# Performance work log

Hardware: AMD Instinct MI355X
Metric: run time of the kernel (lower is better)

Reference implementation:

```python
import jax, jax.numpy as jnp
import numpy as np

B, L, D, H = 8, 512, 1024, 16
HD = D // H  # head dim = 64
SCALE = 1.0  # scale=False in __init__


def _rel_sinusoid(seq_len, dim):
    # RelativeSinusoidalPositionalEmbedding lookup for relative positions
    # arange(-L/2, L/2) (even L), sinusoid of the raw relative position.
    half = dim // 2
    inv = jnp.exp(jnp.arange(half, dtype=jnp.float32) * (-(np.log(10000.0) / (half - 1))))
    r = jnp.arange(-(seq_len // 2), seq_len // 2, dtype=jnp.float32)  # (L,)
    ang = r[:, None] * inv[None, :]  # (L, half)
    return jnp.concatenate([jnp.sin(ang), jnp.cos(ang)], axis=1)  # (L, dim)


def setup_inputs() -> dict:
    key = jax.random.key(0)
    ks = jax.random.split(key, 8)
    s = 0.02
    x = jax.random.normal(ks[0], (B, L, D), jnp.float32)
    mask = jax.random.randint(ks[1], (B, L), 0, 2).astype(jnp.int64)
    mask = mask.at[:, 0].set(1)  # ensure at least one valid key per row
    qmask = jax.random.randint(ks[2], (B, L), 0, 2).astype(jnp.int64)
    w_qkv = jax.random.normal(ks[3], (D, 3 * D), jnp.float32) * s
    w_qkpos = jax.random.normal(ks[4], (HD, 2 * D), jnp.float32) * s
    w_fc = jax.random.normal(ks[5], (D, D), jnp.float32) * s
    b_fc = jnp.zeros((D,), jnp.float32)
    shift = jnp.abs(jax.random.normal(ks[6], (1,), jnp.float32)) + 0.001
    bias = -jnp.abs(jax.random.normal(ks[7], (1,), jnp.float32))
    return dict(x=x, mask=mask, qmask=qmask, w_qkv=w_qkv, w_qkpos=w_qkpos,
                w_fc=w_fc, b_fc=b_fc, shift=shift, bias=bias)


def reference(x, mask, qmask, w_qkv, w_qkpos, w_fc, b_fc, shift, bias):
    # trans_type='self', use_Gaussian=True, dropout in eval mode (identity)
    b, l, d = x.shape
    qkv = x @ w_qkv  # (B, L, 3D)
    q, k, v = jnp.split(qkv, 3, axis=-1)
    q = q.reshape(b, l, H, HD).transpose(0, 2, 1, 3)  # (B,H,L,hd)
    k = k.reshape(b, l, H, HD).transpose(0, 2, 1, 3)
    v = v.reshape(b, l, H, HD).transpose(0, 2, 1, 3)

    pe = _rel_sinusoid(l, HD)               # (L, hd)
    y = pe @ w_qkpos                        # (L, 2D)
    q_p, k_p = jnp.split(y, 2, axis=-1)     # (L, D) each
    q_p = q_p.reshape(l, H, HD).transpose(1, 0, 2)  # (H, L, hd)
    k_p = k_p.reshape(l, H, HD).transpose(1, 0, 2)  # (H, L, hd)

    attn = jnp.einsum('bhid,bhjd->bhij', q, k) + jnp.einsum('hid,hjd->hij', q_p, k_p)[None]

    # speaker-identity masking: zero out cross-speaker scores (trans_type='self')
    qsame = qmask[:, :, None] == qmask[:, None, :]  # (B, L, L)
    attn = jnp.where(qsame[:, None], attn, 0.0)
    attn = attn / SCALE

    # key padding mask -> -inf
    attn = jnp.where(mask[:, None, None, :] == 0, -jnp.inf, attn)

    # Gaussian distance bias: -(shift * (i-j)^2 + bias)
    idx = jnp.arange(l, dtype=jnp.float32)
    sqd = (idx[:, None] - idx[None, :]) ** 2  # (L, L)
    attn = attn + (-(shift[0] * sqd + bias[0]))[None, None]

    attn = jax.nn.softmax(attn, axis=-1)
    out = jnp.einsum('bhij,bhjd->bhid', attn, v)  # (B,H,L,hd)
    out = out.transpose(0, 2, 1, 3).reshape(b, l, d)
    return out @ w_fc + b_fc
```

## Files before the change

### kernel.cpp

```cpp
#include <hip/hip_runtime.h>
#include <hip/hip_bf16.h>

#define BB 8
#define LL 512
#define DD 1024
#define HH 16
#define HD 64
#define LOG2E 1.4426950408889634f

typedef __attribute__((ext_vector_type(8))) unsigned short u16x8;
typedef __attribute__((ext_vector_type(4))) unsigned short u16x4;
typedef __attribute__((ext_vector_type(8))) __bf16 bf16x8;
typedef __attribute__((ext_vector_type(4))) float f32x4;
typedef __attribute__((ext_vector_type(16))) float f32x16;

#define DEV __device__ __forceinline__

DEV unsigned short f2bf(float f) {
    return __builtin_bit_cast(unsigned short, (__bf16)f);
}
DEV f32x4 mfma16(u16x8 a, u16x8 b, f32x4 c) {
    return __builtin_amdgcn_mfma_f32_16x16x32_bf16(
        __builtin_bit_cast(bf16x8, a), __builtin_bit_cast(bf16x8, b), c, 0, 0, 0);
}
DEV f32x16 mfma32(u16x8 a, u16x8 b, f32x16 c) {
    return __builtin_amdgcn_mfma_f32_32x32x16_bf16(
        __builtin_bit_cast(bf16x8, a), __builtin_bit_cast(bf16x8, b), c, 0, 0, 0);
}
typedef __attribute__((address_space(1))) void gv_t;
typedef __attribute__((address_space(3))) void lv_t;
DEV void gload16(const void* g, void* l) {
    __builtin_amdgcn_global_load_lds((gv_t*)g, (lv_t*)l, 16, 0, 0);
}


__global__ __launch_bounds__(256) void cvt_x(const float* __restrict__ in,
                                             unsigned short* __restrict__ out) {
    int i = blockIdx.x * 256 + threadIdx.x;
    f32x4 v = *(const f32x4*)(in + i * 4);
    u16x4 o;
    o[0] = f2bf(v[0]); o[1] = f2bf(v[1]); o[2] = f2bf(v[2]); o[3] = f2bf(v[3]);
    *(u16x4*)(out + i * 4) = o;
}

__global__ __launch_bounds__(256) void transpose_cvt(
    const float* __restrict__ in, unsigned short* __restrict__ out,
    int R, int C) {
    __shared__ unsigned short tile[32][33];
    int c0 = blockIdx.x * 32, r0 = blockIdx.y * 32;
    int tx = threadIdx.x & 31, ty = threadIdx.x >> 5;
#pragma unroll
    for (int i = 0; i < 32; i += 8)
        tile[ty + i][tx] = f2bf(in[(r0 + ty + i) * C + c0 + tx]);
    __syncthreads();
#pragma unroll
    for (int i = 0; i < 32; i += 8)
        out[(c0 + ty + i) * R + r0 + tx] = tile[tx][ty + i];
}

__global__ __launch_bounds__(256) void posg(
    const float* __restrict__ w, unsigned short* __restrict__ qpx,
    unsigned short* __restrict__ kpx) {
    __shared__ float peS[64][64];
    __shared__ float wS[64][32];
    int c0 = blockIdx.x * 32, i0 = blockIdx.y * 64;
    int t = threadIdx.x;
#pragma unroll
    for (int j = 0; j < 16; ++j) {
        int o = t + j * 256;
        int ri = o >> 6, d = o & 63, dd = d & 31;
        float inv = expf((float)dd * -0.2971077539347156f);
        float ang = (float)(i0 + ri - 256) * inv;
        peS[ri][d] = (d < 32) ? sinf(ang) : cosf(ang);
    }
#pragma unroll
    for (int j = 0; j < 8; ++j) {
        int o = t + j * 256;
        wS[o >> 5][o & 31] = w[(o >> 5) * 2048 + c0 + (o & 31)];
    }
    __syncthreads();
#pragma unroll
    for (int j = 0; j < 8; ++j) {
        int o = t + j * 256;
        int row = o >> 5, col = o & 31;
        float acc = 0.0f;
#pragma unroll
        for (int k = 0; k < 64; ++k) acc += peS[row][k] * wS[k][col];
        int c = c0 + col, i = i0 + row;
        int qt = i >> 5, lq = i & 31;
        int cc = (c < 1024) ? c : (c - 1024);
        int h = cc >> 6, kk = cc & 63;
        int ks = kk >> 4, h2 = (kk >> 3) & 1, jj = kk & 7;
        unsigned idx = ((unsigned)(h * 4096 + qt * 256 + ks * 64 + h2 * 32 + lq)
                        << 3) + jj;
        if (c < 1024) qpx[idx] = f2bf(acc * LOG2E);
        else          kpx[idx] = f2bf(acc);
    }
}

template <int MODE>
__global__ __launch_bounds__(256) void gemm_bt(
    const unsigned short* __restrict__ A, const unsigned short* __restrict__ Bt,
    int M, int N, int K, int NBX, unsigned short* __restrict__ o0,
    unsigned short* __restrict__ o1, unsigned short* __restrict__ o2,
    float* __restrict__ fout, const float* __restrict__ bias) {
    __shared__ __align__(16) unsigned short As[2][128 * 32];
    __shared__ __align__(16) unsigned short Bs[2][128 * 32];
    int g = blockIdx.x;
    int swz = (g & 7) * (gridDim.x >> 3) + (g >> 3);
    int bx = swz % NBX, by = swz / NBX;
    int m0 = by * 128, n0 = bx * 128;
    int t = threadIdx.x;
    int w = t >> 6, l = t & 63, lg = l >> 4, lc = l & 15;
    int wr = w >> 1, wc = w & 1;

    f32x4 acc[4][4] = {};

    int sr = t >> 2;
    int sc = (t & 3) ^ ((t >> 3) & 3);
    const unsigned short* Ab = A + (m0 + sr) * K + sc * 8;
    const unsigned short* Bb = Bt + (n0 + sr) * K + sc * 8;
    int rsw = (lc >> 1) & 3;

    auto stage = [&](int buf, int k0) {
        gload16(Ab + k0, &As[buf][w * 512]);
        gload16(Ab + 64 * K + k0, &As[buf][2048 + w * 512]);
        gload16(Bb + k0, &Bs[buf][w * 512]);
        gload16(Bb + 64 * K + k0, &Bs[buf][2048 + w * 512]);
    };

    stage(0, 0);
    stage(1, 32);
    int cur = 0;
    for (int k0 = 0; k0 < K; k0 += 32) {
        if (k0 + 32 < K)
            asm volatile("s_waitcnt vmcnt(4)" ::: "memory");
        else
            asm volatile("s_waitcnt vmcnt(0)" ::: "memory");
        __builtin_amdgcn_sched_barrier(0);
        __builtin_amdgcn_s_barrier();
        __builtin_amdgcn_sched_barrier(0);
        u16x8 af[4], bf[4];
#pragma unroll
        for (int mm = 0; mm < 4; ++mm)
            af[mm] = *(const u16x8*)&As[cur][(wr * 64 + mm * 16 + lc) * 32 +
                                             ((lg ^ rsw) << 3)];
#pragma unroll
        for (int nn = 0; nn < 4; ++nn)
            bf[nn] = *(const u16x8*)&Bs[cur][(wc * 64 + nn * 16 + lc) * 32 +
                                             ((lg ^ rsw) << 3)];
        asm volatile("s_waitcnt lgkmcnt(0)" ::: "memory");
        __builtin_amdgcn_sched_barrier(0);
        __builtin_amdgcn_s_barrier();
        __builtin_amdgcn_sched_barrier(0);
        if (k0 + 64 < K) stage(cur, k0 + 64);
#pragma unroll
        for (int mm = 0; mm < 4; ++mm)
#pragma unroll
            for (int nn = 0; nn < 4; ++nn)
                acc[mm][nn] = mfma16(af[mm], bf[nn], acc[mm][nn]);
        cur ^= 1;
    }

#pragma unroll
    for (int mm = 0; mm < 4; ++mm)
#pragma unroll
        for (int nn = 0; nn < 4; ++nn)
#pragma unroll
            for (int r = 0; r < 4; ++r) {
                int row = m0 + wr * 64 + mm * 16 + lg * 4 + r;
                int col = n0 + wc * 64 + nn * 16 + lc;
                float v = acc[mm][nn][r];
                if (MODE == 0) {
                    int bb = row >> 9, i = row & 511;
                    int which = col >> 10, dd = col & 1023;
                    int hh = dd >> 6, hd = dd & 63;
                    int bh2 = bb * HH + hh;
                    int tl = i >> 5, io = i & 31;
                    if (which == 2) {
                        int h2 = (io >> 2) & 1, ps = (io >> 4) & 1;
                        int j = (io & 3) | (((io >> 3) & 1) << 2);
                        int dblk = hd >> 5, lq = hd & 31;
                        unsigned idx = ((unsigned)(bh2 * 4096 + tl * 256 +
                                        (dblk * 2 + ps) * 64 + h2 * 32 + lq)
                                        << 3) + j;
                        o2[idx] = f2bf(v);
                    } else {
                        int ks = hd >> 4, h2 = (hd >> 3) & 1, j = hd & 7;
                        unsigned idx = ((unsigned)(bh2 * 4096 + tl * 256 +
                                        ks * 64 + h2 * 32 + io) << 3) + j;
                        if (which == 0) o0[idx] = f2bf(v * LOG2E);
                        else            o1[idx] = f2bf(v);
                    }
                } else {
                    fout[row * N + col] = v + bias[col];
                }
            }
}

__global__ void attn_k(
    const unsigned short* __restrict__ Qx, const unsigned short* __restrict__ Kx,
    const unsigned short* __restrict__ Vx, const unsigned short* __restrict__ QPx,
    const unsigned short* __restrict__ KPx, const int* __restrict__ mask,
    const int* __restrict__ qmask, const float* __restrict__ shp,
    unsigned short* __restrict__ out) {
    __shared__ float mbuf[2][64];
    __shared__ float lsbuf[2][64];
    __shared__ float obuf[2][64][33];

    int g = blockIdx.x;
    int bid = ((g & 7) << 7) + (g >> 3);
    int b = bid >> 7, h = (bid >> 3) & 15, qc = bid & 7;
    int t = threadIdx.x, w = t >> 6, l = t & 63;
    int qg = w & 1, kh = w >> 1;
    int lq = l & 31, hi = l >> 5;
    int q = qc * 64 + qg * 32 + lq;
    int bh = b * HH + h;
    int qt = qc * 2 + qg;

    const unsigned short* qb  = Qx  + (((unsigned)(bh * 4096 + qt * 256)) << 3) + (l << 3);
    const unsigned short* qpb = QPx + (((unsigned)(h  * 4096 + qt * 256)) << 3) + (l << 3);
    u16x8 qf[4], pf[4];
#pragma unroll
    for (int ks = 0; ks < 4; ++ks) {
        qf[ks] = *(const u16x8*)(qb + ks * 512);
        pf[ks] = *(const u16x8*)(qpb + ks * 512);
    }

    unsigned long long km[4], qm[4];
#pragma unroll
    for (int t8 = 0; t8 < 4; ++t8) {
        int base = b * LL + (kh * 4 + t8) * 64 + l;
        km[t8] = __ballot(mask[base] != 0);
        qm[t8] = __ballot(qmask[base] != 0);
    }
    int qi = (qmask[b * LL + q] != 0) ? 1 : 0;

    const float M0 = -1.0e30f, NEGF = -3.0e38f, THR = 8.0f;
    float negs = -(*shp) * LOG2E;
    float m = M0, ls = 0.0f;
    f32x16 o0 = {}, o1 = {};
    float fq = (float)(q - 4 * hi);

#pragma unroll
    for (int tt = 0; tt < 8; ++tt) {
        int ttg = kh * 8 + tt;
        const unsigned short* kb  = Kx  + (((unsigned)(bh * 4096 + ttg * 256)) << 3) + (l << 3);
        const unsigned short* kpb = KPx + (((unsigned)(h  * 4096 + ttg * 256)) << 3) + (l << 3);
        const unsigned short* vb  = Vx  + (((unsigned)(bh * 4096 + ttg * 256)) << 3) + (l << 3);
        u16x8 vf0 = *(const u16x8*)(vb);
        u16x8 vf1 = *(const u16x8*)(vb + 512);
        u16x8 vf2 = *(const u16x8*)(vb + 1024);
        u16x8 vf3 = *(const u16x8*)(vb + 1536);
        f32x16 sk = {}, sp = {};
#pragma unroll
        for (int ks = 0; ks < 4; ++ks) {
            sk = mfma32(*(const u16x8*)(kb + ks * 512), qf[ks], sk);
            sp = mfma32(*(const u16x8*)(kpb + ks * 512), pf[ks], sp);
        }

        unsigned kwn = ((unsigned)(km[tt >> 1] >> ((tt & 1) * 32))) >> (hi * 4);
        unsigned qwn = ((unsigned)(qm[tt >> 1] >> ((tt & 1) * 32))) >> (hi * 4);
        float bt = fq - 32.0f * (float)ttg;
        float p[16];
#pragma unroll
        for (int r = 0; r < 16; ++r) {
            const int off = (r & 3) + 8 * (r >> 2);
            float v = sk[r] + sp[r];
            v = (((qwn >> off) & 1u) == (unsigned)qi) ? v : 0.0f;
            float dr = bt - (float)off;
            v = __builtin_fmaf(negs * dr, dr, v);
            v = ((kwn >> off) & 1u) ? v : NEGF;
            p[r] = v;
        }
        float a0 = fmaxf(fmaxf(p[0], p[1]), fmaxf(p[2], p[3]));
        float a1 = fmaxf(fmaxf(p[4], p[5]), fmaxf(p[6], p[7]));
        float a2 = fmaxf(fmaxf(p[8], p[9]), fmaxf(p[10], p[11]));
        float a3 = fmaxf(fmaxf(p[12], p[13]), fmaxf(p[14], p[15]));
        float pmax = fmaxf(fmaxf(a0, a1), fmaxf(a2, a3));
        pmax = fmaxf(pmax, __shfl_xor(pmax, 32));
        if (!__all(pmax <= m + THR)) {
            float mn = fmaxf(m, pmax);
            float sc = __builtin_amdgcn_exp2f(m - mn);
#pragma unroll
            for (int r = 0; r < 16; ++r) { o0[r] *= sc; o1[r] *= sc; }
            ls *= sc;
            m = mn;
        }
#pragma unroll
        for (int r = 0; r < 16; ++r) p[r] = __builtin_amdgcn_exp2f(p[r] - m);
        ls += (((p[0] + p[1]) + (p[2] + p[3])) + ((p[4] + p[5]) + (p[6] + p[7]))) +
              (((p[8] + p[9]) + (p[10] + p[11])) +
               ((p[12] + p[13]) + (p[14] + p[15])));
        u16x8 pf0, pf1;
#pragma unroll
        for (int j = 0; j < 8; ++j) { pf0[j] = f2bf(p[j]); pf1[j] = f2bf(p[8 + j]); }
        o0 = mfma32(vf0, pf0, o0);
        o0 = mfma32(vf1, pf1, o0);
        o1 = mfma32(vf2, pf0, o1);
        o1 = mfma32(vf3, pf1, o1);
    }

    if (kh == 1) {
        mbuf[qg][l] = m;
        lsbuf[qg][l] = ls;
#pragma unroll
        for (int r = 0; r < 16; ++r) {
            obuf[qg][l][r] = o0[r];
            obuf[qg][l][16 + r] = o1[r];
        }
    }
    __syncthreads();
    if (kh == 0) {
        float m1 = mbuf[qg][l], ls1 = lsbuf[qg][l];
        float mm = fmaxf(m, m1);
        float sc0 = __builtin_amdgcn_exp2f(m - mm);
        float sc1 = __builtin_amdgcn_exp2f(m1 - mm);
        float lsm = ls * sc0 + ls1 * sc1;
        float rs = lsm + __shfl_xor(lsm, 32);
        float rinv = __builtin_amdgcn_rcpf(rs);
        unsigned short* ob = out + ((long)(b * LL + q)) * DD + h * HD + hi * 4;
#pragma unroll
        for (int rg = 0; rg < 4; ++rg) {
            u16x4 pk0, pk1;
#pragma unroll
            for (int rr = 0; rr < 4; ++rr) {
                int i = rg * 4 + rr;
                float v0 = __builtin_fmaf(o0[i], sc0, obuf[qg][l][i] * sc1);
                float v1 = __builtin_fmaf(o1[i], sc0, obuf[qg][l][16 + i] * sc1);
                pk0[rr] = f2bf(v0 * rinv);
                pk1[rr] = f2bf(v1 * rinv);
            }
            *(u16x4*)(ob + rg * 8) = pk0;
            *(u16x4*)(ob + 32 + rg * 8) = pk1;
        }
    }
}

extern "C" void kernel_launch(void* const* d_in, const int* in_sizes, int n_in,
                              void* d_out, int out_size, void* d_ws,
                              size_t ws_size, hipStream_t stream) {
    const float* x     = (const float*)d_in[0];
    const int*   mask  = (const int*)d_in[1];
    const int*   qmask = (const int*)d_in[2];
    const float* w_qkv = (const float*)d_in[3];
    const float* w_qkp = (const float*)d_in[4];
    const float* w_fc  = (const float*)d_in[5];
    const float* b_fc  = (const float*)d_in[6];
    const float* shift = (const float*)d_in[7];

    char* ws = (char*)d_ws;
    unsigned short* xb   = (unsigned short*)(ws);
    unsigned short* qb   = (unsigned short*)(ws + 8388608);
    unsigned short* kb   = (unsigned short*)(ws + 16777216);
    unsigned short* vtb  = (unsigned short*)(ws + 25165824);
    unsigned short* qp   = (unsigned short*)(ws + 33554432);
    unsigned short* kp   = (unsigned short*)(ws + 34603008);
    unsigned short* wqt  = (unsigned short*)(ws + 35651584);
    unsigned short* wft  = (unsigned short*)(ws + 41943040);
    unsigned short* aout = (unsigned short*)(ws + 44040192);

    cvt_x<<<4096, 256, 0, stream>>>(x, xb);
    transpose_cvt<<<dim3(96, 32), 256, 0, stream>>>(w_qkv, wqt, 1024, 3072);
    transpose_cvt<<<dim3(32, 32), 256, 0, stream>>>(w_fc, wft, 1024, 1024);
    posg<<<dim3(64, 8), 256, 0, stream>>>(w_qkp, qp, kp);
    gemm_bt<0><<<768, 256, 0, stream>>>(xb, wqt, 4096, 3072, 1024, 24, qb, kb,
                                        vtb, nullptr, nullptr);
    attn_k<<<1024, 256, 0, stream>>>(qb, kb, vtb, qp, kp, mask, qmask, shift,
                                     aout);
    gemm_bt<1><<<256, 256, 0, stream>>>(aout, wft, 4096, 1024, 1024, 8, nullptr,
                                        nullptr, nullptr, (float*)d_out, b_fc);
}
```

Measured before the change: 136.2 us.

## Process two query tiles per wave in attention to reuse K/V loads

Each wave now handles two 32-row query tiles instead of one, so every K, K-positional and V fragment loaded from global memory is used for two score and PV MFMA chains. The grid is halved to 512 blocks and the shared-memory reduction buffers are doubled to hold both tiles' partial softmax states. The aim is to cut redundant global K/V traffic and give the scheduler more independent MFMA work. The cost is higher register pressure, which may lower occupancy, and fewer blocks to spread across CUs.

```diff
diff --git a/kernel.cpp b/kernel.cpp
--- a/kernel.cpp
+++ b/kernel.cpp
@@ -204,27 +204,29 @@
     const unsigned short* __restrict__ KPx, const int* __restrict__ mask,
     const int* __restrict__ qmask, const float* __restrict__ shp,
     unsigned short* __restrict__ out) {
-    __shared__ float mbuf[2][64];
-    __shared__ float lsbuf[2][64];
-    __shared__ float obuf[2][64][33];
+    __shared__ float mbuf[2][2][64];
+    __shared__ float lsbuf[2][2][64];
+    __shared__ float obuf[2][2][64][33];
 
     int g = blockIdx.x;
-    int bid = ((g & 7) << 7) + (g >> 3);
-    int b = bid >> 7, h = (bid >> 3) & 15, qc = bid & 7;
+    int bid = ((g & 7) << 6) + (g >> 3);
+    int b = bid >> 6, h = (bid >> 2) & 15, qq = bid & 3;
     int t = threadIdx.x, w = t >> 6, l = t & 63;
     int qg = w & 1, kh = w >> 1;
     int lq = l & 31, hi = l >> 5;
-    int q = qc * 64 + qg * 32 + lq;
+    int c0 = qq * 4 + qg * 2, c1 = c0 + 1;
+    int qA = c0 * 32 + lq, qB = qA + 32;
     int bh = b * HH + h;
-    int qt = qc * 2 + qg;
-
-    const unsigned short* qb  = Qx  + (((unsigned)(bh * 4096 + qt * 256)) << 3) + (l << 3);
-    const unsigned short* qpb = QPx + (((unsigned)(h  * 4096 + qt * 256)) << 3) + (l << 3);
-    u16x8 qf[4], pf[4];
+
+    const unsigned short* qbA  = Qx  + (((unsigned)(bh * 4096 + c0 * 256)) << 3) + (l << 3);
+    const unsigned short* qpbA = QPx + (((unsigned)(h  * 4096 + c0 * 256)) << 3) + (l << 3);
+    u16x8 qfA[4], pfA[4], qfB[4], pfB[4];
 #pragma unroll
     for (int ks = 0; ks < 4; ++ks) {
-        qf[ks] = *(const u16x8*)(qb + ks * 512);
-        pf[ks] = *(const u16x8*)(qpb + ks * 512);
+        qfA[ks] = *(const u16x8*)(qbA + ks * 512);
+        pfA[ks] = *(const u16x8*)(qpbA + ks * 512);
+        qfB[ks] = *(const u16x8*)(qbA + 2048 + ks * 512);
+        pfB[ks] = *(const u16x8*)(qpbA + 2048 + ks * 512);
     }
 
     unsigned long long km[4], qm[4];
@@ -234,13 +236,15 @@
         km[t8] = __ballot(mask[base] != 0);
         qm[t8] = __ballot(qmask[base] != 0);
     }
-    int qi = (qmask[b * LL + q] != 0) ? 1 : 0;
+    int qiA = (qmask[b * LL + qA] != 0) ? 1 : 0;
+    int qiB = (qmask[b * LL + qB] != 0) ? 1 : 0;
 
     const float M0 = -1.0e30f, NEGF = -3.0e38f, THR = 8.0f;
     float negs = -(*shp) * LOG2E;
-    float m = M0, ls = 0.0f;
-    f32x16 o0 = {}, o1 = {};
-    float fq = (float)(q - 4 * hi);
+    float mA = M0, lsA = 0.0f, mB = M0, lsB = 0.0f;
+    f32x16 oA0 = {}, oA1 = {}, oB0 = {}, oB1 = {};
+    float fqA = (float)(qA - 4 * hi);
+    float fqB = (float)(qB - 4 * hi);
 
 #pragma unroll
     for (int tt = 0; tt < 8; ++tt) {
@@ -248,91 +252,170 @@
         const unsigned short* kb  = Kx  + (((unsigned)(bh * 4096 + ttg * 256)) << 3) + (l << 3);
         const unsigned short* kpb = KPx + (((unsigned)(h  * 4096 + ttg * 256)) << 3) + (l << 3);
         const unsigned short* vb  = Vx  + (((unsigned)(bh * 4096 + ttg * 256)) << 3) + (l << 3);
-        u16x8 vf0 = *(const u16x8*)(vb);
-        u16x8 vf1 = *(const u16x8*)(vb + 512);
-        u16x8 vf2 = *(const u16x8*)(vb + 1024);
-        u16x8 vf3 = *(const u16x8*)(vb + 1536);
-        f32x16 sk = {}, sp = {};
+        u16x8 kf[4], kpf[4], vf[4];
 #pragma unroll
         for (int ks = 0; ks < 4; ++ks) {
-            sk = mfma32(*(const u16x8*)(kb + ks * 512), qf[ks], sk);
-            sp = mfma32(*(const u16x8*)(kpb + ks * 512), pf[ks], sp);
+            kf[ks]  = *(const u16x8*)(kb + ks * 512);
+            kpf[ks] = *(const u16x8*)(kpb + ks * 512);
+            vf[ks]  = *(const u16x8*)(vb + ks * 512);
+        }
+        f32x16 sA = {}, sB = {};
+#pragma unroll
+        for (int ks = 0; ks < 4; ++ks) {
+            sA = mfma32(kf[ks], qfA[ks], sA);
+            sB = mfma32(kf[ks], qfB[ks], sB);
+        }
+#pragma unroll
+        for (int ks = 0; ks < 4; ++ks) {
+            sA = mfma32(kpf[ks], pfA[ks], sA);
+            sB = mfma32(kpf[ks], pfB[ks], sB);
         }
 
         unsigned kwn = ((unsigned)(km[tt >> 1] >> ((tt & 1) * 32))) >> (hi * 4);
         unsigned qwn = ((unsigned)(qm[tt >> 1] >> ((tt & 1) * 32))) >> (hi * 4);
-        float bt = fq - 32.0f * (float)ttg;
-        float p[16];
+        float btA = fqA - 32.0f * (float)ttg;
+        float btB = fqB - 32.0f * (float)ttg;
+
+        {
+            float p[16];
+#pragma unroll
+            for (int r = 0; r < 16; ++r) {
+                const int off = (r & 3) + 8 * (r >> 2);
+                float v = sA[r];
+                v = (((qwn >> off) & 1u) == (unsigned)qiA) ? v : 0.0f;
+                float dr = btA - (float)off;
+                v = __builtin_fmaf(negs * dr, dr, v);
+                v = ((kwn >> off) & 1u) ? v : NEGF;
+                p[r] = v;
+            }
+            float a0 = fmaxf(fmaxf(p[0], p[1]), fmaxf(p[2], p[3]));
+            float a1 = fmaxf(fmaxf(p[4], p[5]), fmaxf(p[6], p[7]));
+            float a2 = fmaxf(fmaxf(p[8], p[9]), fmaxf(p[10], p[11]));
+            float a3 = fmaxf(fmaxf(p[12], p[13]), fmaxf(p[14], p[15]));
+            float pmax = fmaxf(fmaxf(a0, a1), fmaxf(a2, a3));
+            pmax = fmaxf(pmax, __shfl_xor(pmax, 32));
+            if (!__all(pmax <= mA + THR)) {
+                float mn = fmaxf(mA, pmax);
+                float sc = __builtin_amdgcn_exp2f(mA - mn);
+#pragma unroll
+                for (int r = 0; r < 16; ++r) { oA0[r] *= sc; oA1[r] *= sc; }
+                lsA *= sc;
+                mA = mn;
+            }
+#pragma unroll
+            for (int r = 0; r < 16; ++r) p[r] = __builtin_amdgcn_exp2f(p[r] - mA);
+            lsA += (((p[0] + p[1]) + (p[2] + p[3])) + ((p[4] + p[5]) + (p[6] + p[7]))) +
+                   (((p[8] + p[9]) + (p[10] + p[11])) +
+                    ((p[12] + p[13]) + (p[14] + p[15])));
+            u16x8 pf0, pf1;
+#pragma unroll
+            for (int j = 0; j < 8; ++j) { pf0[j] = f2bf(p[j]); pf1[j] = f2bf(p[8 + j]); }
+            oA0 = mfma32(vf[0], pf0, oA0);
+            oA0 = mfma32(vf[1], pf1, oA0);
+            oA1 = mfma32(vf[2], pf0, oA1);
+            oA1 = mfma32(vf[3], pf1, oA1);
+        }
+        {
+            float p[16];
+#pragma unroll
+            for (int r = 0; r < 16; ++r) {
+                const int off = (r & 3) + 8 * (r >> 2);
+                float v = sB[r];
+                v = (((qwn >> off) & 1u) == (unsigned)qiB) ? v : 0.0f;
+                float dr = btB - (float)off;
+                v = __builtin_fmaf(negs * dr, dr, v);
+                v = ((kwn >> off) & 1u) ? v : NEGF;
+                p[r] = v;
+            }
+            float a0 = fmaxf(fmaxf(p[0], p[1]), fmaxf(p[2], p[3]));
+            float a1 = fmaxf(fmaxf(p[4], p[5]), fmaxf(p[6], p[7]));
+            float a2 = fmaxf(fmaxf(p[8], p[9]), fmaxf(p[10], p[11]));
+            float a3 = fmaxf(fmaxf(p[12], p[13]), fmaxf(p[14], p[15]));
+            float pmax = fmaxf(fmaxf(a0, a1), fmaxf(a2, a3));
+            pmax = fmaxf(pmax, __shfl_xor(pmax, 32));
+            if (!__all(pmax <= mB + THR)) {
+                float mn = fmaxf(mB, pmax);
+                float sc = __builtin_amdgcn_exp2f(mB - mn);
+#pragma unroll
+                for (int r = 0; r < 16; ++r) { oB0[r] *= sc; oB1[r] *= sc; }
+                lsB *= sc;
+                mB = mn;
+            }
+#pragma unroll
+            for (int r = 0; r < 16; ++r) p[r] = __builtin_amdgcn_exp2f(p[r] - mB);
+            lsB += (((p[0] + p[1]) + (p[2] + p[3])) + ((p[4] + p[5]) + (p[6] + p[7]))) +
+                   (((p[8] + p[9]) + (p[10] + p[11])) +
+                    ((p[12] + p[13]) + (p[14] + p[15])));
+            u16x8 pf0, pf1;
+#pragma unroll
+            for (int j = 0; j < 8; ++j) { pf0[j] = f2bf(p[j]); pf1[j] = f2bf(p[8 + j]); }
+            oB0 = mfma32(vf[0], pf0, oB0);
+            oB0 = mfma32(vf[1], pf1, oB0);
+            oB1 = mfma32(vf[2], pf0, oB1);
+            oB1 = mfma32(vf[3], pf1, oB1);
+        }
+    }
+
+    if (kh == 1) {
+        mbuf[qg][0][l] = mA;  lsbuf[qg][0][l] = lsA;
+        mbuf[qg][1][l] = mB;  lsbuf[qg][1][l] = lsB;
 #pragma unroll
         for (int r = 0; r < 16; ++r) {
-            const int off = (r & 3) + 8 * (r >> 2);
-            float v = sk[r] + sp[r];
-            v = (((qwn >> off) & 1u) == (unsigned)qi) ? v : 0.0f;
-            float dr = bt - (float)off;
-            v = __builtin_fmaf(negs * dr, dr, v);
-            v = ((kwn >> off) & 1u) ? v : NEGF;
-            p[r] = v;
-        }
-        float a0 = fmaxf(fmaxf(p[0], p[1]), fmaxf(p[2], p[3]));
-        float a1 = fmaxf(fmaxf(p[4], p[5]), fmaxf(p[6], p[7]));
-        float a2 = fmaxf(fmaxf(p[8], p[9]), fmaxf(p[10], p[11]));
-        float a3 = fmaxf(fmaxf(p[12], p[13]), fmaxf(p[14], p[15]));
-        float pmax = fmaxf(fmaxf(a0, a1), fmaxf(a2, a3));
-        pmax = fmaxf(pmax, __shfl_xor(pmax, 32));
-        if (!__all(pmax <= m + THR)) {
-            float mn = fmaxf(m, pmax);
-            float sc = __builtin_amdgcn_exp2f(m - mn);
-#pragma unroll
-            for (int r = 0; r < 16; ++r) { o0[r] *= sc; o1[r] *= sc; }
-            ls *= sc;
-            m = mn;
-        }
-#pragma unroll
-        for (int r = 0; r < 16; ++r) p[r] = __builtin_amdgcn_exp2f(p[r] - m);
-        ls += (((p[0] + p[1]) + (p[2] + p[3])) + ((p[4] + p[5]) + (p[6] + p[7]))) +
-              (((p[8] + p[9]) + (p[10] + p[11])) +
-               ((p[12] + p[13]) + (p[14] + p[15])));
-        u16x8 pf0, pf1;
-#pragma unroll
-        for (int j = 0; j < 8; ++j) { pf0[j] = f2bf(p[j]); pf1[j] = f2bf(p[8 + j]); }
-        o0 = mfma32(vf0, pf0, o0);
-        o0 = mfma32(vf1, pf1, o0);
-        o1 = mfma32(vf2, pf0, o1);
-        o1 = mfma32(vf3, pf1, o1);
-    }
-
-    if (kh == 1) {
-        mbuf[qg][l] = m;
-        lsbuf[qg][l] = ls;
-#pragma unroll
-        for (int r = 0; r < 16; ++r) {
-            obuf[qg][l][r] = o0[r];
-            obuf[qg][l][16 + r] = o1[r];
+            obuf[qg][0][l][r] = oA0[r];
+            obuf[qg][0][l][16 + r] = oA1[r];
+            obuf[qg][1][l][r] = oB0[r];
+            obuf[qg][1][l][16 + r] = oB1[r];
         }
     }
     __syncthreads();
     if (kh == 0) {
-        float m1 = mbuf[qg][l], ls1 = lsbuf[qg][l];
-        float mm = fmaxf(m, m1);
-        float sc0 = __builtin_amdgcn_exp2f(m - mm);
-        float sc1 = __builtin_amdgcn_exp2f(m1 - mm);
-        float lsm = ls * sc0 + ls1 * sc1;
-        float rs = lsm + __shfl_xor(lsm, 32);
-        float rinv = __builtin_amdgcn_rcpf(rs);
-        unsigned short* ob = out + ((long)(b * LL + q)) * DD + h * HD + hi * 4;
-#pragma unroll
-        for (int rg = 0; rg < 4; ++rg) {
-            u16x4 pk0, pk1;
-#pragma unroll
-            for (int rr = 0; rr < 4; ++rr) {
-                int i = rg * 4 + rr;
-                float v0 = __builtin_fmaf(o0[i], sc0, obuf[qg][l][i] * sc1);
-                float v1 = __builtin_fmaf(o1[i], sc0, obuf[qg][l][16 + i] * sc1);
-                pk0[rr] = f2bf(v0 * rinv);
-                pk1[rr] = f2bf(v1 * rinv);
-            }
-            *(u16x4*)(ob + rg * 8) = pk0;
-            *(u16x4*)(ob + 32 + rg * 8) = pk1;
+        {
+            float m1 = mbuf[qg][0][l], ls1 = lsbuf[qg][0][l];
+            float mm = fmaxf(mA, m1);
+            float sc0 = __builtin_amdgcn_exp2f(mA - mm);
+            float sc1 = __builtin_amdgcn_exp2f(m1 - mm);
+            float lsm = lsA * sc0 + ls1 * sc1;
+            float rs = lsm + __shfl_xor(lsm, 32);
+            float rinv = __builtin_amdgcn_rcpf(rs);
+            unsigned short* ob = out + ((long)(b * LL + qA)) * DD + h * HD + hi * 4;
+#pragma unroll
+            for (int rg = 0; rg < 4; ++rg) {
+                u16x4 pk0, pk1;
+#pragma unroll
+                for (int rr = 0; rr < 4; ++rr) {
+                    int i = rg * 4 + rr;
+                    float v0 = __builtin_fmaf(oA0[i], sc0, obuf[qg][0][l][i] * sc1);
+                    float v1 = __builtin_fmaf(oA1[i], sc0, obuf[qg][0][l][16 + i] * sc1);
+                    pk0[rr] = f2bf(v0 * rinv);
+                    pk1[rr] = f2bf(v1 * rinv);
+                }
+                *(u16x4*)(ob + rg * 8) = pk0;
+                *(u16x4*)(ob + 32 + rg * 8) = pk1;
+            }
+        }
+        {
+            float m1 = mbuf[qg][1][l], ls1 = lsbuf[qg][1][l];
+            float mm = fmaxf(mB, m1);
+            float sc0 = __builtin_amdgcn_exp2f(mB - mm);
+            float sc1 = __builtin_amdgcn_exp2f(m1 - mm);
+            float lsm = lsB * sc0 + ls1 * sc1;
+            float rs = lsm + __shfl_xor(lsm, 32);
+            float rinv = __builtin_amdgcn_rcpf(rs);
+            unsigned short* ob = out + ((long)(b * LL + qB)) * DD + h * HD + hi * 4;
+#pragma unroll
+            for (int rg = 0; rg < 4; ++rg) {
+                u16x4 pk0, pk1;
+#pragma unroll
+                for (int rr = 0; rr < 4; ++rr) {
+                    int i = rg * 4 + rr;
+                    float v0 = __builtin_fmaf(oB0[i], sc0, obuf[qg][1][l][i] * sc1);
+                    float v1 = __builtin_fmaf(oB1[i], sc0, obuf[qg][1][l][16 + i] * sc1);
+                    pk0[rr] = f2bf(v0 * rinv);
+                    pk1[rr] = f2bf(v1 * rinv);
+                }
+                *(u16x4*)(ob + rg * 8) = pk0;
+                *(u16x4*)(ob + 32 + rg * 8) = pk1;
+            }
         }
     }
 }
@@ -366,8 +449,8 @@
     posg<<<dim3(64, 8), 256, 0, stream>>>(w_qkp, qp, kp);
     gemm_bt<0><<<768, 256, 0, stream>>>(xb, wqt, 4096, 3072, 1024, 24, qb, kb,
                                         vtb, nullptr, nullptr);
-    attn_k<<<1024, 256, 0, stream>>>(qb, kb, vtb, qp, kp, mask, qmask, shift,
-                                     aout);
+    attn_k<<<512, 256, 0, stream>>>(qb, kb, vtb, qp, kp, mask, qmask, shift,
+                                    aout);
     gemm_bt<1><<<256, 256, 0, stream>>>(aout, wft, 4096, 1024, 1024, 8, nullptr,
                                         nullptr, nullptr, (float*)d_out, b_fc);
 }
```

New measurement: 203.0 us. +49.1%, slower.
